# Kernel tuning notes

Measured on AMD Instinct MI355X. Metric: run time of the kernel, lower is better.

Reference implementation:

```python
import jax, jax.numpy as jnp
import numpy as np

B, N, U = 16, 1024, 64  # batch, nodes, num_units
ALPHA = 0.2  # LeakyReLU negative slope
NEG = -9e15


def setup_inputs() -> dict:
    key = jax.random.key(0)
    ks = jax.random.split(key, 7)
    X = jax.random.normal(ks[0], (B, N, U), dtype=jnp.float32)
    state = jax.random.normal(ks[1], (B, N, U), dtype=jnp.float32)
    # random sparse adjacency (avg degree ~32) with self-loops
    adj = (jax.random.uniform(ks[2], (N, N)) < 32.0 / N).astype(jnp.float32)
    adj = jnp.maximum(adj, jnp.eye(N, dtype=jnp.float32))
    def xavier(k, shape):
        fan_in, fan_out = shape
        s = 1.414 * np.sqrt(6.0 / (fan_in + fan_out))
        return jax.random.uniform(k, shape, jnp.float32, -s, s)
    W1 = xavier(ks[3], (2 * U, 2 * U))   # gat_1: in 2U -> out 2U
    a1 = xavier(ks[4], (4 * U, 1))       # attention vector, 2*out
    W2 = xavier(ks[5], (2 * U, U))       # gat_2: in 2U -> out U
    a2 = xavier(ks[6], (2 * U, 1))
    return {"X": X, "state": state, "adj": adj, "W1": W1, "a1": a1, "W2": W2, "a2": a2}


def _gat_layer(x, adj, W, a):
    # x: [b,n,f_in], W: [f_in,F], a: [2F,1]
    h = jnp.einsum('bnf,fo->bno', x, W)              # [b,n,F]
    F_out = W.shape[1]
    s_src = h @ a[:F_out, 0]                         # [b,n] contribution of node i
    s_dst = h @ a[F_out:, 0]                         # [b,n] contribution of node j
    e = jax.nn.leaky_relu(s_src[:, :, None] + s_dst[:, None, :], ALPHA)  # [b,n,n]
    e = jnp.where(adj[None, :, :] > 0, e, NEG)
    att = jax.nn.softmax(e, axis=2)                  # masked softmax over neighbors j
    return jnp.einsum('bij,bjf->bif', att, h)        # [b,n,F]


def reference(X, state, adj, W1, a1, W2, a2):
    X1 = jnp.concatenate([X, state], axis=2)         # [b,n,2U]
    gv = jax.nn.sigmoid(_gat_layer(X1, adj, W1, a1)) # [b,n,2U]
    r, z = jnp.split(gv, 2, axis=2)                  # each [b,n,U]
    X2 = jnp.concatenate([X, r * state], axis=2)
    h_t1 = jnp.tanh(_gat_layer(X2, adj, W2, a2))     # [b,n,U]
    new_h = z * state + (1.0 - z) * h_t1
    return new_h
```

## Files before the change

kernel.cpp:

```cpp
#include <hip/hip_runtime.h>

#define BB 16
#define NN 1024
#define LALPHA 0.2f
#define MAXD 192

__global__ void build_csr(const float* __restrict__ adj, int* __restrict__ deg,
                          int* __restrict__ cols) {
    __shared__ int cnt;
    int i = blockIdx.x;
    if (threadIdx.x == 0) cnt = 0;
    __syncthreads();
    for (int j = threadIdx.x; j < NN; j += blockDim.x) {
        if (adj[(size_t)i * NN + j] > 0.0f) {
            int p = atomicAdd(&cnt, 1);
            if (p < MAXD) cols[(size_t)i * MAXD + p] = j;
        }
    }
    __syncthreads();
    if (threadIdx.x == 0) deg[i] = cnt < MAXD ? cnt : MAXD;
}

template <int FOUT, int RB>
__global__ void gemm_score(const float* __restrict__ A0, const float* __restrict__ A1,
                           const float* __restrict__ W, const float* __restrict__ avec,
                           float* __restrict__ h, float* __restrict__ s_src,
                           float* __restrict__ s_dst) {
    constexpr int TFN = FOUT / 4;
    constexpr int NT = (RB / 4) * TFN;
    __shared__ float xs[RB][132];
    int t = threadIdx.x;
    int tf = t % TFN, tr = t / TFN;
    int f0 = tf * 4, r0 = tr * 4;
    int base = blockIdx.x * RB;

    for (int idx = t; idx < RB * 32; idx += NT) {
        int r = idx >> 5, c = (idx & 31) * 4;
        float4 v = (c < 64) ? *(const float4*)(A0 + (size_t)(base + r) * 64 + c)
                            : *(const float4*)(A1 + (size_t)(base + r) * 64 + (c - 64));
        xs[r][c] = v.x; xs[r][c + 1] = v.y; xs[r][c + 2] = v.z; xs[r][c + 3] = v.w;
    }
    __syncthreads();

    float acc[4][4] = {};
    for (int k = 0; k < 128; k += 4) {
        float4 xv[4], wv[4];
#pragma unroll
        for (int i = 0; i < 4; i++) xv[i] = *(const float4*)&xs[r0 + i][k];
#pragma unroll
        for (int i = 0; i < 4; i++) wv[i] = *(const float4*)(W + (size_t)(k + i) * FOUT + f0);
#pragma unroll
        for (int i = 0; i < 4; i++) {
            float xr[4] = {xv[i].x, xv[i].y, xv[i].z, xv[i].w};
#pragma unroll
            for (int kk = 0; kk < 4; kk++) {
                acc[i][0] += xr[kk] * wv[kk].x;
                acc[i][1] += xr[kk] * wv[kk].y;
                acc[i][2] += xr[kk] * wv[kk].z;
                acc[i][3] += xr[kk] * wv[kk].w;
            }
        }
    }

    float a_s[4], a_d[4];
#pragma unroll
    for (int i = 0; i < 4; i++) {
        a_s[i] = avec[f0 + i];
        a_d[i] = avec[FOUT + f0 + i];
    }
#pragma unroll
    for (int i = 0; i < 4; i++) {
        int m = base + r0 + i;
        *(float4*)(h + (size_t)m * FOUT + f0) =
            make_float4(acc[i][0], acc[i][1], acc[i][2], acc[i][3]);
        float ps = acc[i][0] * a_s[0] + acc[i][1] * a_s[1] + acc[i][2] * a_s[2] + acc[i][3] * a_s[3];
        float pd = acc[i][0] * a_d[0] + acc[i][1] * a_d[1] + acc[i][2] * a_d[2] + acc[i][3] * a_d[3];
#pragma unroll
        for (int o = TFN / 2; o >= 1; o >>= 1) {
            ps += __shfl_xor(ps, o);
            pd += __shfl_xor(pd, o);
        }
        if (tf == 0) {
            s_src[m] = ps;
            s_dst[m] = pd;
        }
    }
}

__global__ void attn1_kernel(const int* __restrict__ deg, const int* __restrict__ cols,
                             const float* __restrict__ h1, const float* __restrict__ s_src,
                             const float* __restrict__ s_dst, const float* __restrict__ state,
                             float* __restrict__ rstate, float* __restrict__ zbuf) {
    int bi = blockIdx.x;
    int i = bi & (NN - 1);
    int b = bi >> 10;
    int lane = threadIdx.x;
    int d = deg[i];
    float ssrc = s_src[bi];
    __shared__ float w[MAXD];
    __shared__ int cl[MAXD];
    for (int j = lane; j < d; j += 64) cl[j] = cols[(size_t)i * MAXD + j];
    __syncthreads();
    float mx = -1e30f;
    for (int j = lane; j < d; j += 64) {
        float e = ssrc + s_dst[b * NN + cl[j]];
        e = e > 0.f ? e : LALPHA * e;
        w[j] = e;
        mx = fmaxf(mx, e);
    }
#pragma unroll
    for (int o = 32; o >= 1; o >>= 1) mx = fmaxf(mx, __shfl_xor(mx, o));
    float sum = 0.f;
    for (int j = lane; j < d; j += 64) {
        float e = __expf(w[j] - mx);
        w[j] = e;
        sum += e;
    }
#pragma unroll
    for (int o = 32; o >= 1; o >>= 1) sum += __shfl_xor(sum, o);
    __syncthreads();
    float inv = 1.f / sum;
    float acc0 = 0.f, acc1 = 0.f;
    int j = 0;
    for (; j + 1 < d; j += 2) {
        float w0 = w[j], w1 = w[j + 1];
        const float* p0 = h1 + (size_t)(b * NN + cl[j]) * 128;
        const float* p1 = h1 + (size_t)(b * NN + cl[j + 1]) * 128;
        float x0 = p0[lane], y0 = p0[lane + 64];
        float x1 = p1[lane], y1 = p1[lane + 64];
        acc0 += w0 * x0 + w1 * x1;
        acc1 += w0 * y0 + w1 * y1;
    }
    if (j < d) {
        float w0 = w[j];
        const float* p0 = h1 + (size_t)(b * NN + cl[j]) * 128;
        acc0 += w0 * p0[lane];
        acc1 += w0 * p0[lane + 64];
    }
    float rg = 1.f / (1.f + __expf(-acc0 * inv));
    float zg = 1.f / (1.f + __expf(-acc1 * inv));
    float st = state[(size_t)bi * 64 + lane];
    rstate[(size_t)bi * 64 + lane] = rg * st;
    zbuf[(size_t)bi * 64 + lane] = zg;
}

__global__ void attn2_kernel(const int* __restrict__ deg, const int* __restrict__ cols,
                             const float* __restrict__ h2, const float* __restrict__ s_src,
                             const float* __restrict__ s_dst, const float* __restrict__ state,
                             const float* __restrict__ zbuf, float* __restrict__ out) {
    int bi = blockIdx.x;
    int i = bi & (NN - 1);
    int b = bi >> 10;
    int lane = threadIdx.x;
    int d = deg[i];
    float ssrc = s_src[bi];
    __shared__ float w[MAXD];
    __shared__ int cl[MAXD];
    for (int j = lane; j < d; j += 64) cl[j] = cols[(size_t)i * MAXD + j];
    __syncthreads();
    float mx = -1e30f;
    for (int j = lane; j < d; j += 64) {
        float e = ssrc + s_dst[b * NN + cl[j]];
        e = e > 0.f ? e : LALPHA * e;
        w[j] = e;
        mx = fmaxf(mx, e);
    }
#pragma unroll
    for (int o = 32; o >= 1; o >>= 1) mx = fmaxf(mx, __shfl_xor(mx, o));
    float sum = 0.f;
    for (int j = lane; j < d; j += 64) {
        float e = __expf(w[j] - mx);
        w[j] = e;
        sum += e;
    }
#pragma unroll
    for (int o = 32; o >= 1; o >>= 1) sum += __shfl_xor(sum, o);
    __syncthreads();
    float inv = 1.f / sum;
    float acc = 0.f;
    int j = 0;
    for (; j + 1 < d; j += 2) {
        float w0 = w[j], w1 = w[j + 1];
        const float* p0 = h2 + (size_t)(b * NN + cl[j]) * 64;
        const float* p1 = h2 + (size_t)(b * NN + cl[j + 1]) * 64;
        acc += w0 * p0[lane] + w1 * p1[lane];
    }
    if (j < d) acc += w[j] * h2[(size_t)(b * NN + cl[j]) * 64 + lane];
    float ht = tanhf(acc * inv);
    float z = zbuf[(size_t)bi * 64 + lane];
    float st = state[(size_t)bi * 64 + lane];
    out[(size_t)bi * 64 + lane] = z * st + (1.f - z) * ht;
}

extern "C" void kernel_launch(void* const* d_in, const int* in_sizes, int n_in,
                              void* d_out, int out_size, void* d_ws, size_t ws_size,
                              hipStream_t stream) {
    const float* X     = (const float*)d_in[0];
    const float* state = (const float*)d_in[1];
    const float* adj   = (const float*)d_in[2];
    const float* W1    = (const float*)d_in[3];
    const float* a1    = (const float*)d_in[4];
    const float* W2    = (const float*)d_in[5];
    const float* a2    = (const float*)d_in[6];
    float* out = (float*)d_out;

    char* ws = (char*)d_ws;
    size_t off = 0;
    auto alloc = [&](size_t bytes) -> void* {
        void* p = ws + off;
        off = (off + bytes + 255) & ~(size_t)255;
        return p;
    };
    int*   deg    = (int*)alloc(NN * sizeof(int));
    int*   cols   = (int*)alloc((size_t)NN * MAXD * sizeof(int));
    float* h1     = (float*)alloc((size_t)BB * NN * 128 * sizeof(float));
    float* ssrc1  = (float*)alloc((size_t)BB * NN * sizeof(float));
    float* sdst1  = (float*)alloc((size_t)BB * NN * sizeof(float));
    float* rstate = (float*)alloc((size_t)BB * NN * 64 * sizeof(float));
    float* zbuf   = (float*)alloc((size_t)BB * NN * 64 * sizeof(float));
    float* h2     = (float*)alloc((size_t)BB * NN * 64 * sizeof(float));
    float* ssrc2  = (float*)alloc((size_t)BB * NN * sizeof(float));
    float* sdst2  = (float*)alloc((size_t)BB * NN * sizeof(float));

    const int M = BB * NN;

    build_csr<<<NN, 256, 0, stream>>>(adj, deg, cols);
    gemm_score<128, 32><<<M / 32, 256, 0, stream>>>(X, state, W1, a1, h1, ssrc1, sdst1);
    attn1_kernel<<<M, 64, 0, stream>>>(deg, cols, h1, ssrc1, sdst1, state, rstate, zbuf);
    gemm_score<64, 64><<<M / 64, 256, 0, stream>>>(X, rstate, W2, a2, h2, ssrc2, sdst2);
    attn2_kernel<<<M, 64, 0, stream>>>(deg, cols, h2, ssrc2, sdst2, state, zbuf, out);
}
```

Before: 142.3 us.

## Fuse second-layer projection into attention-1 and vectorize neighbor gathers with float4

Attention-1 now computes r*state and z, assembles the [X, r*state] row in shared memory, and directly does the 128x64 projection with W2 plus both attention scores. This removes the rstate buffer round trip and the separate second GEMM launch. Both aggregation loops are changed to float4 gathers, with half-waves or quarter-waves handling different neighbors and a shuffle reduction at the end. The trade-off is that W2 is re-read per node through scalar loads without reuse, instead of being tiled.

```diff
diff --git a/kernel.cpp b/kernel.cpp
--- a/kernel.cpp
+++ b/kernel.cpp
@@ -87,10 +87,108 @@
     }
 }
 
-__global__ void attn1_kernel(const int* __restrict__ deg, const int* __restrict__ cols,
-                             const float* __restrict__ h1, const float* __restrict__ s_src,
-                             const float* __restrict__ s_dst, const float* __restrict__ state,
-                             float* __restrict__ rstate, float* __restrict__ zbuf) {
+__global__ __launch_bounds__(64) void attn1_fused(
+    const int* __restrict__ deg, const int* __restrict__ cols,
+    const float* __restrict__ h1, const float* __restrict__ s_src,
+    const float* __restrict__ s_dst, const float* __restrict__ state,
+    const float* __restrict__ X, const float* __restrict__ W2,
+    const float* __restrict__ a2, float* __restrict__ zbuf,
+    float* __restrict__ h2, float* __restrict__ ssrc2, float* __restrict__ sdst2) {
+    int bi = blockIdx.x;
+    int i = bi & (NN - 1);
+    int b = bi >> 10;
+    int lane = threadIdx.x;
+    int d = deg[i];
+    float ssrc = s_src[bi];
+    __shared__ float w[MAXD];
+    __shared__ int cl[MAXD];
+    __shared__ float x2[128];
+    for (int j = lane; j < d; j += 64) cl[j] = cols[(size_t)i * MAXD + j];
+    __syncthreads();
+    float mx = -1e30f;
+    for (int j = lane; j < d; j += 64) {
+        float e = ssrc + s_dst[b * NN + cl[j]];
+        e = e > 0.f ? e : LALPHA * e;
+        w[j] = e;
+        mx = fmaxf(mx, e);
+    }
+#pragma unroll
+    for (int o = 32; o >= 1; o >>= 1) mx = fmaxf(mx, __shfl_xor(mx, o));
+    float sum = 0.f;
+    for (int j = lane; j < d; j += 64) {
+        float e = __expf(w[j] - mx);
+        w[j] = e;
+        sum += e;
+    }
+#pragma unroll
+    for (int o = 32; o >= 1; o >>= 1) sum += __shfl_xor(sum, o);
+    __syncthreads();
+    float inv = 1.f / sum;
+
+    int half = lane >> 5, fl = lane & 31;
+    const float* hb = h1 + (size_t)b * NN * 128;
+    float4 acc = make_float4(0.f, 0.f, 0.f, 0.f);
+    for (int j = 0; j < d; j += 2) {
+        int jj = j + half;
+        float wt = (jj < d) ? w[jj] : 0.f;
+        int row = cl[(jj < d) ? jj : j];
+        float4 v = *(const float4*)(hb + (size_t)row * 128 + fl * 4);
+        acc.x += wt * v.x; acc.y += wt * v.y; acc.z += wt * v.z; acc.w += wt * v.w;
+    }
+    acc.x += __shfl_xor(acc.x, 32);
+    acc.y += __shfl_xor(acc.y, 32);
+    acc.z += __shfl_xor(acc.z, 32);
+    acc.w += __shfl_xor(acc.w, 32);
+
+    size_t mo = (size_t)bi * 64;
+    if (lane < 16) {
+        float4 st = *(const float4*)(state + mo + lane * 4);
+        float4 rs;
+        rs.x = st.x / (1.f + __expf(-acc.x * inv));
+        rs.y = st.y / (1.f + __expf(-acc.y * inv));
+        rs.z = st.z / (1.f + __expf(-acc.z * inv));
+        rs.w = st.w / (1.f + __expf(-acc.w * inv));
+        *(float4*)&x2[64 + lane * 4] = rs;
+    } else if (lane < 32) {
+        float4 z;
+        z.x = 1.f / (1.f + __expf(-acc.x * inv));
+        z.y = 1.f / (1.f + __expf(-acc.y * inv));
+        z.z = 1.f / (1.f + __expf(-acc.z * inv));
+        z.w = 1.f / (1.f + __expf(-acc.w * inv));
+        *(float4*)(zbuf + mo + (lane - 16) * 4) = z;
+    } else if (lane < 48) {
+        *(float4*)&x2[(lane - 32) * 4] = *(const float4*)(X + mo + (lane - 32) * 4);
+    }
+    __syncthreads();
+
+    float hacc = 0.f;
+#pragma unroll 8
+    for (int k = 0; k < 128; k += 4) {
+        float4 xv = *(const float4*)&x2[k];
+        hacc += xv.x * W2[(size_t)(k + 0) * 64 + lane];
+        hacc += xv.y * W2[(size_t)(k + 1) * 64 + lane];
+        hacc += xv.z * W2[(size_t)(k + 2) * 64 + lane];
+        hacc += xv.w * W2[(size_t)(k + 3) * 64 + lane];
+    }
+    h2[mo + lane] = hacc;
+    float ps = hacc * a2[lane];
+    float pd = hacc * a2[64 + lane];
+#pragma unroll
+    for (int o = 32; o >= 1; o >>= 1) {
+        ps += __shfl_xor(ps, o);
+        pd += __shfl_xor(pd, o);
+    }
+    if (lane == 0) {
+        ssrc2[bi] = ps;
+        sdst2[bi] = pd;
+    }
+}
+
+__global__ __launch_bounds__(64) void attn2_kernel(
+    const int* __restrict__ deg, const int* __restrict__ cols,
+    const float* __restrict__ h2, const float* __restrict__ s_src,
+    const float* __restrict__ s_dst, const float* __restrict__ state,
+    const float* __restrict__ zbuf, float* __restrict__ out) {
     int bi = blockIdx.x;
     int i = bi & (NN - 1);
     int b = bi >> 10;
@@ -120,76 +218,37 @@
     for (int o = 32; o >= 1; o >>= 1) sum += __shfl_xor(sum, o);
     __syncthreads();
     float inv = 1.f / sum;
-    float acc0 = 0.f, acc1 = 0.f;
-    int j = 0;
-    for (; j + 1 < d; j += 2) {
-        float w0 = w[j], w1 = w[j + 1];
-        const float* p0 = h1 + (size_t)(b * NN + cl[j]) * 128;
-        const float* p1 = h1 + (size_t)(b * NN + cl[j + 1]) * 128;
-        float x0 = p0[lane], y0 = p0[lane + 64];
-        float x1 = p1[lane], y1 = p1[lane + 64];
-        acc0 += w0 * x0 + w1 * x1;
-        acc1 += w0 * y0 + w1 * y1;
-    }
-    if (j < d) {
-        float w0 = w[j];
-        const float* p0 = h1 + (size_t)(b * NN + cl[j]) * 128;
-        acc0 += w0 * p0[lane];
-        acc1 += w0 * p0[lane + 64];
-    }
-    float rg = 1.f / (1.f + __expf(-acc0 * inv));
-    float zg = 1.f / (1.f + __expf(-acc1 * inv));
-    float st = state[(size_t)bi * 64 + lane];
-    rstate[(size_t)bi * 64 + lane] = rg * st;
-    zbuf[(size_t)bi * 64 + lane] = zg;
-}
-
-__global__ void attn2_kernel(const int* __restrict__ deg, const int* __restrict__ cols,
-                             const float* __restrict__ h2, const float* __restrict__ s_src,
-                             const float* __restrict__ s_dst, const float* __restrict__ state,
-                             const float* __restrict__ zbuf, float* __restrict__ out) {
-    int bi = blockIdx.x;
-    int i = bi & (NN - 1);
-    int b = bi >> 10;
-    int lane = threadIdx.x;
-    int d = deg[i];
-    float ssrc = s_src[bi];
-    __shared__ float w[MAXD];
-    __shared__ int cl[MAXD];
-    for (int j = lane; j < d; j += 64) cl[j] = cols[(size_t)i * MAXD + j];
-    __syncthreads();
-    float mx = -1e30f;
-    for (int j = lane; j < d; j += 64) {
-        float e = ssrc + s_dst[b * NN + cl[j]];
-        e = e > 0.f ? e : LALPHA * e;
-        w[j] = e;
-        mx = fmaxf(mx, e);
-    }
-#pragma unroll
-    for (int o = 32; o >= 1; o >>= 1) mx = fmaxf(mx, __shfl_xor(mx, o));
-    float sum = 0.f;
-    for (int j = lane; j < d; j += 64) {
-        float e = __expf(w[j] - mx);
-        w[j] = e;
-        sum += e;
-    }
-#pragma unroll
-    for (int o = 32; o >= 1; o >>= 1) sum += __shfl_xor(sum, o);
-    __syncthreads();
-    float inv = 1.f / sum;
-    float acc = 0.f;
-    int j = 0;
-    for (; j + 1 < d; j += 2) {
-        float w0 = w[j], w1 = w[j + 1];
-        const float* p0 = h2 + (size_t)(b * NN + cl[j]) * 64;
-        const float* p1 = h2 + (size_t)(b * NN + cl[j + 1]) * 64;
-        acc += w0 * p0[lane] + w1 * p1[lane];
-    }
-    if (j < d) acc += w[j] * h2[(size_t)(b * NN + cl[j]) * 64 + lane];
-    float ht = tanhf(acc * inv);
-    float z = zbuf[(size_t)bi * 64 + lane];
-    float st = state[(size_t)bi * 64 + lane];
-    out[(size_t)bi * 64 + lane] = z * st + (1.f - z) * ht;
+
+    int q = lane >> 4, fl = lane & 15;
+    const float* hb = h2 + (size_t)b * NN * 64;
+    float4 acc = make_float4(0.f, 0.f, 0.f, 0.f);
+    for (int j = 0; j < d; j += 4) {
+        int jj = j + q;
+        float wt = (jj < d) ? w[jj] : 0.f;
+        int row = cl[(jj < d) ? jj : j];
+        float4 v = *(const float4*)(hb + (size_t)row * 64 + fl * 4);
+        acc.x += wt * v.x; acc.y += wt * v.y; acc.z += wt * v.z; acc.w += wt * v.w;
+    }
+    acc.x += __shfl_xor(acc.x, 32);
+    acc.y += __shfl_xor(acc.y, 32);
+    acc.z += __shfl_xor(acc.z, 32);
+    acc.w += __shfl_xor(acc.w, 32);
+    acc.x += __shfl_xor(acc.x, 16);
+    acc.y += __shfl_xor(acc.y, 16);
+    acc.z += __shfl_xor(acc.z, 16);
+    acc.w += __shfl_xor(acc.w, 16);
+
+    if (lane < 16) {
+        size_t mo = (size_t)bi * 64;
+        float4 z = *(const float4*)(zbuf + mo + lane * 4);
+        float4 st = *(const float4*)(state + mo + lane * 4);
+        float4 o4;
+        o4.x = z.x * st.x + (1.f - z.x) * tanhf(acc.x * inv);
+        o4.y = z.y * st.y + (1.f - z.y) * tanhf(acc.y * inv);
+        o4.z = z.z * st.z + (1.f - z.z) * tanhf(acc.z * inv);
+        o4.w = z.w * st.w + (1.f - z.w) * tanhf(acc.w * inv);
+        *(float4*)(out + mo + lane * 4) = o4;
+    }
 }
 
 extern "C" void kernel_launch(void* const* d_in, const int* in_sizes, int n_in,
@@ -216,7 +275,6 @@
     float* h1     = (float*)alloc((size_t)BB * NN * 128 * sizeof(float));
     float* ssrc1  = (float*)alloc((size_t)BB * NN * sizeof(float));
     float* sdst1  = (float*)alloc((size_t)BB * NN * sizeof(float));
-    float* rstate = (float*)alloc((size_t)BB * NN * 64 * sizeof(float));
     float* zbuf   = (float*)alloc((size_t)BB * NN * 64 * sizeof(float));
     float* h2     = (float*)alloc((size_t)BB * NN * 64 * sizeof(float));
     float* ssrc2  = (float*)alloc((size_t)BB * NN * sizeof(float));
@@ -226,7 +284,7 @@
 
     build_csr<<<NN, 256, 0, stream>>>(adj, deg, cols);
     gemm_score<128, 32><<<M / 32, 256, 0, stream>>>(X, state, W1, a1, h1, ssrc1, sdst1);
-    attn1_kernel<<<M, 64, 0, stream>>>(deg, cols, h1, ssrc1, sdst1, state, rstate, zbuf);
-    gemm_score<64, 64><<<M / 64, 256, 0, stream>>>(X, rstate, W2, a2, h2, ssrc2, sdst2);
+    attn1_fused<<<M, 64, 0, stream>>>(deg, cols, h1, ssrc1, sdst1, state, X, W2, a2,
+                                      zbuf, h2, ssrc2, sdst2);
     attn2_kernel<<<M, 64, 0, stream>>>(deg, cols, h2, ssrc2, sdst2, state, zbuf, out);
 }
```

Result: faster. 137.5 us (-3.4%).
